# Performance work log

Hardware: AMD Instinct MI355X
Metric: run time of the kernel (lower is better)

## Reference

```python
import jax, jax.numpy as jnp
import numpy as np

B, T, C = 8, 4096, 384
H, F = 6, 64          # heads, head_size; H*F == C
E = 131072            # edges per graph (shared across batch)
D_FF = 4 * C
NEG_SLOPE = 0.2       # PyG GATConv LeakyReLU slope
EPS = 1e-5


def layer_norm(x, g, b):
    mu = jnp.mean(x, axis=-1, keepdims=True)
    var = jnp.mean(jnp.square(x - mu), axis=-1, keepdims=True)
    return (x - mu) * jax.lax.rsqrt(var + EPS) * g + b


def setup_inputs() -> dict:
    key = jax.random.key(0)
    ks = jax.random.split(key, 14)
    s = 0.02
    return {
        "x": jax.random.normal(ks[0], (B, T, C), dtype=jnp.float32),
        "edge_index": jax.random.randint(ks[1], (2, E), 0, T, dtype=jnp.int32),
        "W_gat": jax.random.normal(ks[2], (C, H * F), dtype=jnp.float32) * s,
        "att_src": jax.random.normal(ks[3], (H, F), dtype=jnp.float32) * s,
        "att_dst": jax.random.normal(ks[4], (H, F), dtype=jnp.float32) * s,
        "b_gat": jnp.zeros((C,), dtype=jnp.float32),
        "ln1_g": jnp.ones((C,), dtype=jnp.float32),
        "ln1_b": jnp.zeros((C,), dtype=jnp.float32),
        "ln2_g": jnp.ones((C,), dtype=jnp.float32),
        "ln2_b": jnp.zeros((C,), dtype=jnp.float32),
        "W1": jax.random.normal(ks[5], (C, D_FF), dtype=jnp.float32) * s,
        "b1": jnp.zeros((D_FF,), dtype=jnp.float32),
        "W2": jax.random.normal(ks[6], (D_FF, C), dtype=jnp.float32) * s,
        "b2": jnp.zeros((C,), dtype=jnp.float32),
    }


def reference(x, edge_index, W_gat, att_src, att_dst, b_gat,
              ln1_g, ln1_b, ln2_g, ln2_b, W1, b1, W2, b2):
    # PyG GATConv adds self-loops by default
    loop = jnp.arange(T, dtype=edge_index.dtype)
    src = jnp.concatenate([edge_index[0], loop])  # [E+T]
    dst = jnp.concatenate([edge_index[1], loop])  # [E+T]

    def gat_single(xn):  # xn: [T, C] (already layer-normed)
        h = (xn @ W_gat).reshape(T, H, F)                      # [T,H,F]
        a_src = jnp.einsum('thf,hf->th', h, att_src)           # [T,H]
        a_dst = jnp.einsum('thf,hf->th', h, att_dst)           # [T,H]
        alpha = a_src[src] + a_dst[dst]                        # [E+T,H]
        alpha = jnp.where(alpha >= 0, alpha, NEG_SLOPE * alpha)
        # segment softmax over incoming edges of each dst node
        m = jax.ops.segment_max(alpha, dst, num_segments=T)    # [T,H]
        ex = jnp.exp(alpha - m[dst])
        denom = jax.ops.segment_sum(ex, dst, num_segments=T)   # [T,H]
        w = ex / denom[dst]                                    # [E+T,H]
        msg = w[:, :, None] * h[src]                           # [E+T,H,F]
        out = jax.ops.segment_sum(msg, dst, num_segments=T)    # [T,H,F]
        return out.reshape(T, H * F) + b_gat

    out = jax.vmap(gat_single)(layer_norm(x, ln1_g, ln1_b))    # [B,T,C]
    x = x + out                                                # dropout in eval mode = identity
    h = layer_norm(x, ln2_g, ln2_b)
    x = x + (jnp.maximum(h @ W1 + b1, 0.0) @ W2 + b2)
    return x
```

## Files before the change

### kernel.cpp

```cpp
#include <hip/hip_runtime.h>
#include <hip/hip_bf16.h>

#define Bb 8
#define Tt 4096
#define Cc 384
#define Hh 6
#define Ee 131072
#define DFF 1536
#define NROWS (Bb * Tt)
#define NEG_SLOPE 0.2f

typedef short bf16x8 __attribute__((ext_vector_type(8)));
typedef float f32x4 __attribute__((ext_vector_type(4)));

__device__ inline float bf2f(unsigned short u) {
    union { unsigned int i; float f; } x; x.i = ((unsigned int)u) << 16; return x.f;
}
__device__ inline unsigned short f2bf(float f) {
    union { float f; unsigned int i; } x; x.f = f;
    unsigned int r = x.i + 0x7fffu + ((x.i >> 16) & 1u);
    return (unsigned short)(r >> 16);
}
__device__ __forceinline__ float blo(unsigned int u) {
    union { unsigned int i; float f; } x; x.i = u << 16; return x.f;
}
__device__ __forceinline__ float bhi(unsigned int u) {
    union { unsigned int i; float f; } x; x.i = u & 0xffff0000u; return x.f;
}

__device__ __forceinline__ void gl_lds16(const unsigned short* g, unsigned short* l) {
    __builtin_amdgcn_global_load_lds(
        (const __attribute__((address_space(1))) unsigned int*)g,
        (__attribute__((address_space(3))) unsigned int*)l,
        16, 0, 0);
}

__global__ __launch_bounds__(256) void ln_bf16_kernel(const float* __restrict__ x,
                                                      const float* __restrict__ g,
                                                      const float* __restrict__ b,
                                                      unsigned short* __restrict__ y) {
    int row = blockIdx.x * 4 + (threadIdx.x >> 6);
    int lane = threadIdx.x & 63;
    const float* xr = x + (size_t)row * Cc;
    float v[6]; float sum = 0.f, sq = 0.f;
#pragma unroll
    for (int j = 0; j < 6; j++) { float t = xr[j * 64 + lane]; v[j] = t; sum += t; sq += t * t; }
#pragma unroll
    for (int off = 1; off < 64; off <<= 1) { sum += __shfl_xor(sum, off); sq += __shfl_xor(sq, off); }
    float mu = sum * (1.f / 384.f);
    float var = sq * (1.f / 384.f) - mu * mu;
    float rs = rsqrtf(var + 1e-5f);
    unsigned short* yr = y + (size_t)row * Cc;
#pragma unroll
    for (int j = 0; j < 6; j++) { int c = j * 64 + lane; yr[c] = f2bf((v[j] - mu) * rs * g[c] + b[c]); }
}

__global__ __launch_bounds__(256) void transpose_bf16_kernel(const float* __restrict__ W,
                                                             unsigned short* __restrict__ Wt,
                                                             int K, int N) {
    __shared__ float t[32][33];
    const int n0 = blockIdx.x * 32, k0 = blockIdx.y * 32;
    const int tx = threadIdx.x & 31, ty = threadIdx.x >> 5;
#pragma unroll
    for (int dy = 0; dy < 32; dy += 8)
        t[ty + dy][tx] = W[(size_t)(k0 + ty + dy) * N + n0 + tx];
    __syncthreads();
#pragma unroll
    for (int dy = 0; dy < 32; dy += 8)
        Wt[(size_t)(n0 + ty + dy) * K + k0 + tx] = f2bf(t[tx][ty + dy]);
}

__global__ __launch_bounds__(256) void att_kernel(const unsigned short* __restrict__ h,
                                                  const float* __restrict__ att_src,
                                                  const float* __restrict__ att_dst,
                                                  float* __restrict__ asrc,
                                                  float* __restrict__ adst) {
    int row = blockIdx.x * 4 + (threadIdx.x >> 6);
    int lane = threadIdx.x & 63;
    const unsigned short* hr = h + (size_t)row * Cc;
#pragma unroll
    for (int j = 0; j < 6; j++) {
        float v = bf2f(hr[j * 64 + lane]);
        float ps = v * att_src[j * 64 + lane];
        float pd = v * att_dst[j * 64 + lane];
#pragma unroll
        for (int off = 1; off < 64; off <<= 1) { ps += __shfl_xor(ps, off); pd += __shfl_xor(pd, off); }
        if (lane == 0) { asrc[row * Hh + j] = ps; adst[row * Hh + j] = pd; }
    }
}

__global__ void count_kernel(const int* __restrict__ dst, int* __restrict__ deg) {
    int e = blockIdx.x * 256 + threadIdx.x;
    if (e < Ee) atomicAdd(&deg[dst[e]], 1);
}

__global__ __launch_bounds__(1024) void scan_kernel(int* __restrict__ deg_cursor,
                                                    int* __restrict__ rowptr) {
    __shared__ int lds[1024];
    int tid = threadIdx.x;
    int base_i = tid * 4;
    int v[4];
#pragma unroll
    for (int i = 0; i < 4; i++) v[i] = deg_cursor[base_i + i];
    int s = v[0] + v[1] + v[2] + v[3];
    lds[tid] = s;
    __syncthreads();
    for (int off = 1; off < 1024; off <<= 1) {
        int t = 0;
        if (tid >= off) t = lds[tid - off];
        __syncthreads();
        lds[tid] += t;
        __syncthreads();
    }
    int incl = lds[tid];
    int excl = incl - s;
    int r = excl;
#pragma unroll
    for (int i = 0; i < 4; i++) { rowptr[base_i + i] = r; deg_cursor[base_i + i] = r; r += v[i]; }
    if (tid == 1023) rowptr[Tt] = incl;
}

__global__ void scatter_kernel(const int* __restrict__ src, const int* __restrict__ dst,
                               int* __restrict__ cursor, int* __restrict__ csr) {
    int e = blockIdx.x * 256 + threadIdx.x;
    if (e < Ee) {
        int d = dst[e];
        int pos = atomicAdd(&cursor[d], 1);
        csr[pos] = src[e];
    }
}

__global__ __launch_bounds__(256) void gat_kernel(const unsigned short* __restrict__ h,
                                                  const float* __restrict__ asrc,
                                                  const float* __restrict__ adst,
                                                  const int* __restrict__ rowptr,
                                                  const int* __restrict__ csr,
                                                  const float* __restrict__ x,
                                                  const float* __restrict__ bgat,
                                                  const float* __restrict__ ln2g,
                                                  const float* __restrict__ ln2b,
                                                  float* __restrict__ x2,
                                                  unsigned short* __restrict__ xn) {
    __shared__ float lds_ex[4][64 * 6];
    const int wave = threadIdx.x >> 6;
    const int gid = blockIdx.x * 4 + wave;
    const int lane = threadIdx.x & 63;
    const int b = gid >> 12;
    const int t = gid & (Tt - 1);
    const int bt = b * Tt;
    const bool hihalf = (lane & 32) != 0;
    const int wsel = hihalf ? 1 : 0;
    float* exbuf = lds_ex[wave];

    float adst_j[6];
    {
        const float2* adp = (const float2*)(adst + gid * Hh);
        float2 d01 = adp[0], d23 = adp[1], d45 = adp[2];
        adst_j[0] = d01.x; adst_j[1] = d01.y; adst_j[2] = d23.x;
        adst_j[3] = d23.y; adst_j[4] = d45.x; adst_j[5] = d45.y;
    }

    float den[6], exs[6];
    {
        const float2* asp = (const float2*)(asrc + gid * Hh);
        float2 s01 = asp[0], s23 = asp[1], s45 = asp[2];
        float as_[6] = {s01.x, s01.y, s23.x, s23.y, s45.x, s45.y};
#pragma unroll
        for (int j = 0; j < 6; j++) {
            float a = as_[j] + adst_j[j];
            a = (a >= 0.f) ? a : NEG_SLOPE * a;
            exs[j] = __expf(a);
            den[j] = (lane == 0) ? exs[j] : 0.f;
        }
    }
    float acc[3][2];
    {
        const unsigned short* hs = h + (size_t)gid * Cc;
#pragma unroll
        for (int k = 0; k < 3; k++) {
            unsigned int u = *(const unsigned int*)(hs + k * 128 + 2 * lane);
            float w = exs[2 * k + wsel];
            acc[k][0] = w * blo(u);
            acc[k][1] = w * bhi(u);
        }
    }

    const int e0 = rowptr[t], e1 = rowptr[t + 1];
    for (int c0 = e0; c0 < e1; c0 += 64) {
        const int e = c0 + lane;
        const bool valid = e < e1;
        const int s = csr[valid ? e : (e1 - 1)];
        const int nb = bt + s;
        float ex[6];
        {
            const float2* ap = (const float2*)(asrc + nb * Hh);
            float2 a01 = ap[0], a23 = ap[1], a45 = ap[2];
            float al[6] = {a01.x, a01.y, a23.x, a23.y, a45.x, a45.y};
#pragma unroll
            for (int j = 0; j < 6; j++) {
                float a = al[j] + adst_j[j];
                a = (a >= 0.f) ? a : NEG_SLOPE * a;
                float exx = __expf(a);
                ex[j] = valid ? exx : 0.f;
                den[j] += ex[j];
            }
        }
        *(float2*)&exbuf[lane * 6 + 0] = make_float2(ex[0], ex[1]);
        *(float2*)&exbuf[lane * 6 + 2] = make_float2(ex[2], ex[3]);
        *(float2*)&exbuf[lane * 6 + 4] = make_float2(ex[4], ex[5]);

        const int cnt = (e1 - c0 < 64) ? (e1 - c0) : 64;
        int l2 = 0;
        for (; l2 + 8 <= cnt; l2 += 8) {
            unsigned int u[8][3];
#pragma unroll
            for (int q = 0; q < 8; q++) {
                const int sb = __builtin_amdgcn_readlane(s, l2 + q);
                const unsigned short* hr = h + (size_t)(bt + sb) * Cc + 2 * lane;
                u[q][0] = *(const unsigned int*)(hr);
                u[q][1] = *(const unsigned int*)(hr + 128);
                u[q][2] = *(const unsigned int*)(hr + 256);
            }
#pragma unroll
            for (int q = 0; q < 8; q++) {
                const int e6 = (l2 + q) * 6 + wsel;
                const float w0 = exbuf[e6];
                const float w1 = exbuf[e6 + 2];
                const float w2 = exbuf[e6 + 4];
                acc[0][0] = fmaf(w0, blo(u[q][0]), acc[0][0]);
                acc[0][1] = fmaf(w0, bhi(u[q][0]), acc[0][1]);
                acc[1][0] = fmaf(w1, blo(u[q][1]), acc[1][0]);
                acc[1][1] = fmaf(w1, bhi(u[q][1]), acc[1][1]);
                acc[2][0] = fmaf(w2, blo(u[q][2]), acc[2][0]);
                acc[2][1] = fmaf(w2, bhi(u[q][2]), acc[2][1]);
            }
        }
        for (; l2 < cnt; l2++) {
            const int sb = __builtin_amdgcn_readlane(s, l2);
            const unsigned short* hr = h + (size_t)(bt + sb) * Cc + 2 * lane;
            unsigned int u0 = *(const unsigned int*)(hr);
            unsigned int u1 = *(const unsigned int*)(hr + 128);
            unsigned int u2 = *(const unsigned int*)(hr + 256);
            const int e6 = l2 * 6 + wsel;
            const float w0 = exbuf[e6];
            const float w1 = exbuf[e6 + 2];
            const float w2 = exbuf[e6 + 4];
            acc[0][0] = fmaf(w0, blo(u0), acc[0][0]);
            acc[0][1] = fmaf(w0, bhi(u0), acc[0][1]);
            acc[1][0] = fmaf(w1, blo(u1), acc[1][0]);
            acc[1][1] = fmaf(w1, bhi(u1), acc[1][1]);
            acc[2][0] = fmaf(w2, blo(u2), acc[2][0]);
            acc[2][1] = fmaf(w2, bhi(u2), acc[2][1]);
        }
    }

#pragma unroll
    for (int j = 0; j < 6; j++)
#pragma unroll
        for (int off = 1; off < 64; off <<= 1) den[j] += __shfl_xor(den[j], off);

    float2 ov[3];
#pragma unroll
    for (int k = 0; k < 3; k++) {
        float d = hihalf ? den[2 * k + 1] : den[2 * k];
        float inv = 1.0f / d;
        const int chan = k * 128 + 2 * lane;
        const size_t idx = (size_t)gid * Cc + chan;
        const float2 bg = *(const float2*)(bgat + chan);
        const float2 xv = *(const float2*)(x + idx);
        ov[k].x = fmaf(acc[k][0], inv, bg.x + xv.x);
        ov[k].y = fmaf(acc[k][1], inv, bg.y + xv.y);
        *(float2*)(x2 + idx) = ov[k];
    }
    float sum = 0.f, sq = 0.f;
#pragma unroll
    for (int k = 0; k < 3; k++) {
        sum += ov[k].x + ov[k].y;
        sq += ov[k].x * ov[k].x + ov[k].y * ov[k].y;
    }
#pragma unroll
    for (int off = 1; off < 64; off <<= 1) { sum += __shfl_xor(sum, off); sq += __shfl_xor(sq, off); }
    const float mu = sum * (1.f / 384.f);
    const float var = sq * (1.f / 384.f) - mu * mu;
    const float rs = rsqrtf(var + 1e-5f);
#pragma unroll
    for (int k = 0; k < 3; k++) {
        const int chan = k * 128 + 2 * lane;
        const size_t idx = (size_t)gid * Cc + chan;
        const float2 gg = *(const float2*)(ln2g + chan);
        const float2 bb = *(const float2*)(ln2b + chan);
        float y0 = (ov[k].x - mu) * rs * gg.x + bb.x;
        float y1 = (ov[k].y - mu) * rs * gg.y + bb.y;
        unsigned int pack = (unsigned int)f2bf(y0) | ((unsigned int)f2bf(y1) << 16);
        *(unsigned int*)(xn + idx) = pack;
    }
}

template <int EPI>
__global__ __launch_bounds__(256, 3) void mfma_gemm(const unsigned short* __restrict__ A,
                                                    const unsigned short* __restrict__ Bt,
                                                    const float* __restrict__ bias,
                                                    const float* __restrict__ resid,
                                                    void* __restrict__ Cout,
                                                    int M, int N, int K) {
    __shared__ unsigned short Als[2 * 128 * 32];
    __shared__ unsigned short Bls[2 * 128 * 32];
    const int tid = threadIdx.x;
    const int wave = tid >> 6, lane = tid & 63;
    const int quad = lane >> 4, l16 = lane & 15;
    const int wm = (wave >> 1) * 64, wn = (wave & 1) * 64;
    const int bm = blockIdx.y, bn = blockIdx.x;

    const int c0 = wave * 2;
    const int rowin = lane >> 2;
    const int kel = (lane & 3) * 8;

    const unsigned short* ga = A + (size_t)(bm * 128 + c0 * 16 + rowin) * K + kel;
    const unsigned short* gb = Bt + (size_t)(bn * 128 + c0 * 16 + rowin) * K + kel;
    unsigned short* la = Als + c0 * 512;
    unsigned short* lb = Bls + c0 * 512;

    f32x4 acc[4][4] = {};

    for (int k0 = 0; k0 < K; k0 += 64) {
        gl_lds16(ga + k0, la);
        gl_lds16(ga + k0 + (size_t)16 * K, la + 512);
        gl_lds16(ga + k0 + 32, la + 4096);
        gl_lds16(ga + k0 + (size_t)16 * K + 32, la + 4096 + 512);
        gl_lds16(gb + k0, lb);
        gl_lds16(gb + k0 + (size_t)16 * K, lb + 512);
        gl_lds16(gb + k0 + 32, lb + 4096);
        gl_lds16(gb + k0 + (size_t)16 * K + 32, lb + 4096 + 512);
        __syncthreads();
#pragma unroll
        for (int hh = 0; hh < 2; hh++) {
            bf16x8 af[4], bfr[4];
#pragma unroll
            for (int i = 0; i < 4; i++) {
                af[i]  = *(const bf16x8*)(Als + hh * 4096 + (wm + i * 16 + l16) * 32 + quad * 8);
                bfr[i] = *(const bf16x8*)(Bls + hh * 4096 + (wn + i * 16 + l16) * 32 + quad * 8);
            }
#pragma unroll
            for (int i = 0; i < 4; i++)
#pragma unroll
                for (int j = 0; j < 4; j++)
                    acc[i][j] = __builtin_amdgcn_mfma_f32_16x16x32_bf16(af[i], bfr[j], acc[i][j], 0, 0, 0);
        }
        __syncthreads();
    }

    const int gm = bm * 128 + wm + quad * 4;
    const int gn = bn * 128 + wn + l16;
#pragma unroll
    for (int i = 0; i < 4; i++) {
#pragma unroll
        for (int j = 0; j < 4; j++) {
            const int col = gn + j * 16;
            const float bv = (EPI == 1 || EPI == 2) ? bias[col] : 0.f;
#pragma unroll
            for (int r = 0; r < 4; r++) {
                const int row = gm + i * 16 + r;
                float v = acc[i][j][r] + bv;
                if constexpr (EPI == 1) {
                    ((unsigned short*)Cout)[(size_t)row * N + col] = f2bf(fmaxf(v, 0.f));
                } else if constexpr (EPI == 2) {
                    ((float*)Cout)[(size_t)row * N + col] = v + resid[(size_t)row * N + col];
                } else if constexpr (EPI == 3) {
                    ((unsigned short*)Cout)[(size_t)row * N + col] = f2bf(v);
                } else {
                    ((float*)Cout)[(size_t)row * N + col] = v;
                }
            }
        }
    }
}

extern "C" void kernel_launch(void* const* d_in, const int* in_sizes, int n_in,
                              void* d_out, int out_size, void* d_ws, size_t ws_size,
                              hipStream_t stream) {
    (void)in_sizes; (void)n_in; (void)out_size; (void)ws_size;
    const float* x      = (const float*)d_in[0];
    const int*   ei     = (const int*)d_in[1];
    const float* Wgat   = (const float*)d_in[2];
    const float* attsrc = (const float*)d_in[3];
    const float* attdst = (const float*)d_in[4];
    const float* bgat   = (const float*)d_in[5];
    const float* ln1g   = (const float*)d_in[6];
    const float* ln1b   = (const float*)d_in[7];
    const float* ln2g   = (const float*)d_in[8];
    const float* ln2b   = (const float*)d_in[9];
    const float* W1     = (const float*)d_in[10];
    const float* b1     = (const float*)d_in[11];
    const float* W2     = (const float*)d_in[12];
    const float* b2     = (const float*)d_in[13];
    float* out = (float*)d_out;

    const int* srcp = ei;
    const int* dstp = ei + Ee;

    char* p = (char*)d_ws;
    unsigned short* xn = (unsigned short*)p; p += (size_t)NROWS * Cc * 2;
    unsigned short* h = (unsigned short*)p; p += (size_t)NROWS * Cc * 2;
    float* asrc = (float*)p; p += (size_t)NROWS * Hh * 4;
    float* adst = (float*)p; p += (size_t)NROWS * Hh * 4;
    unsigned short* ffn1 = (unsigned short*)p; p += (size_t)NROWS * DFF * 2;
    unsigned short* wgt = (unsigned short*)p; p += (size_t)Cc * Cc * 2;
    unsigned short* w1t = (unsigned short*)p; p += (size_t)DFF * Cc * 2;
    unsigned short* w2t = (unsigned short*)p; p += (size_t)Cc * DFF * 2;
    int* rowptr = (int*)p; p += (Tt + 1) * 4;
    int* cursor = (int*)p; p += Tt * 4;
    int* csr = (int*)p; p += (size_t)Ee * 4;

    transpose_bf16_kernel<<<dim3(Cc / 32, Cc / 32), 256, 0, stream>>>(Wgat, wgt, Cc, Cc);
    transpose_bf16_kernel<<<dim3(DFF / 32, Cc / 32), 256, 0, stream>>>(W1, w1t, Cc, DFF);
    transpose_bf16_kernel<<<dim3(Cc / 32, DFF / 32), 256, 0, stream>>>(W2, w2t, DFF, Cc);

    hipMemsetAsync(cursor, 0, Tt * sizeof(int), stream);
    count_kernel<<<(Ee + 255) / 256, 256, 0, stream>>>(dstp, cursor);
    scan_kernel<<<1, 1024, 0, stream>>>(cursor, rowptr);
    scatter_kernel<<<(Ee + 255) / 256, 256, 0, stream>>>(srcp, dstp, cursor, csr);

    ln_bf16_kernel<<<NROWS / 4, 256, 0, stream>>>(x, ln1g, ln1b, xn);
    mfma_gemm<3><<<dim3(Cc / 128, NROWS / 128), 256, 0, stream>>>(
        xn, wgt, nullptr, nullptr, h, NROWS, Cc, Cc);
    att_kernel<<<NROWS / 4, 256, 0, stream>>>(h, attsrc, attdst, asrc, adst);
    gat_kernel<<<NROWS / 4, 256, 0, stream>>>(h, asrc, adst, rowptr, csr, x, bgat,
                                              ln2g, ln2b, out, xn);
    mfma_gemm<1><<<dim3(DFF / 128, NROWS / 128), 256, 0, stream>>>(
        xn, w1t, b1, nullptr, ffn1, NROWS, DFF, Cc);
    mfma_gemm<2><<<dim3(Cc / 128, NROWS / 128), 256, 0, stream>>>(
        ffn1, w2t, b2, out, out, NROWS, Cc, DFF);
}
```

Measured before the change: 414.4 us.

## Fold attention projections into LN1 and process two nodes per wave in GAT

Precomputes W_gat·att_src/att_dst into a 384x12 matrix so the attention logits come out of the first layer-norm kernel, which removes the separate att_kernel pass over h. The GAT aggregation kernel now gives each half-wave one destination node, so a wave handles two nodes. Each iteration issues gathers for both nodes' neighbour rows, meant to raise memory-level parallelism and halve the wave count. The trade-offs are wasted lanes when the two nodes' degrees differ, and logits computed from bf16 LN output rather than from bf16 h, a small numerical difference.

```diff
diff --git a/kernel.cpp b/kernel.cpp
--- a/kernel.cpp
+++ b/kernel.cpp
@@ -35,6 +35,74 @@
         16, 0, 0);
 }
 
+__global__ void wcomb_kernel(const float* __restrict__ Wgat,
+                             const float* __restrict__ att_src,
+                             const float* __restrict__ att_dst,
+                             float* __restrict__ Wcomb) {
+    int t = blockIdx.x * 256 + threadIdx.x;
+    if (t >= 384 * 12) return;
+    int k = t / 12, j = t % 12;
+    int hd = j % 6;
+    const float* av = (j < 6 ? att_src : att_dst) + hd * 64;
+    const float* wr = Wgat + (size_t)k * Cc + hd * 64;
+    float acc = 0.f;
+#pragma unroll 8
+    for (int f = 0; f < 64; f++) acc = fmaf(wr[f], av[f], acc);
+    Wcomb[k * 12 + j] = acc;
+}
+
+__global__ __launch_bounds__(256) void ln1_att_kernel(const float* __restrict__ x,
+                                                      const float* __restrict__ g,
+                                                      const float* __restrict__ b,
+                                                      const float* __restrict__ Wcomb,
+                                                      unsigned short* __restrict__ y,
+                                                      float* __restrict__ asrc,
+                                                      float* __restrict__ adst) {
+    int row = blockIdx.x * 4 + (threadIdx.x >> 6);
+    int lane = threadIdx.x & 63;
+    const float* xr = x + (size_t)row * Cc;
+    float v[6]; float sum = 0.f, sq = 0.f;
+#pragma unroll
+    for (int j = 0; j < 6; j++) { float t = xr[j * 64 + lane]; v[j] = t; sum += t; sq += t * t; }
+#pragma unroll
+    for (int off = 1; off < 64; off <<= 1) { sum += __shfl_xor(sum, off); sq += __shfl_xor(sq, off); }
+    float mu = sum * (1.f / 384.f);
+    float var = sq * (1.f / 384.f) - mu * mu;
+    float rs = rsqrtf(var + 1e-5f);
+    unsigned short* yr = y + (size_t)row * Cc;
+    float p[12];
+#pragma unroll
+    for (int jj = 0; jj < 12; jj++) p[jj] = 0.f;
+#pragma unroll
+    for (int j = 0; j < 6; j++) {
+        int c = j * 64 + lane;
+        float yv = (v[j] - mu) * rs * g[c] + b[c];
+        unsigned short ub = f2bf(yv);
+        yr[c] = ub;
+        float yq = bf2f(ub);
+        const float4* w = (const float4*)(Wcomb + c * 12);
+        float4 w0 = w[0], w1 = w[1], w2 = w[2];
+        p[0] = fmaf(yq, w0.x, p[0]); p[1] = fmaf(yq, w0.y, p[1]);
+        p[2] = fmaf(yq, w0.z, p[2]); p[3] = fmaf(yq, w0.w, p[3]);
+        p[4] = fmaf(yq, w1.x, p[4]); p[5] = fmaf(yq, w1.y, p[5]);
+        p[6] = fmaf(yq, w1.z, p[6]); p[7] = fmaf(yq, w1.w, p[7]);
+        p[8] = fmaf(yq, w2.x, p[8]); p[9] = fmaf(yq, w2.y, p[9]);
+        p[10] = fmaf(yq, w2.z, p[10]); p[11] = fmaf(yq, w2.w, p[11]);
+    }
+#pragma unroll
+    for (int off = 1; off < 64; off <<= 1)
+#pragma unroll
+        for (int jj = 0; jj < 12; jj++) p[jj] += __shfl_xor(p[jj], off);
+    if (lane == 0) {
+        float* as_ = asrc + row * Hh;
+        float* ad_ = adst + row * Hh;
+        as_[0] = p[0]; as_[1] = p[1]; as_[2] = p[2];
+        as_[3] = p[3]; as_[4] = p[4]; as_[5] = p[5];
+        ad_[0] = p[6]; ad_[1] = p[7]; ad_[2] = p[8];
+        ad_[3] = p[9]; ad_[4] = p[10]; ad_[5] = p[11];
+    }
+}
+
 __global__ __launch_bounds__(256) void ln_bf16_kernel(const float* __restrict__ x,
                                                       const float* __restrict__ g,
                                                       const float* __restrict__ b,
@@ -68,25 +136,6 @@
 #pragma unroll
     for (int dy = 0; dy < 32; dy += 8)
         Wt[(size_t)(n0 + ty + dy) * K + k0 + tx] = f2bf(t[tx][ty + dy]);
-}
-
-__global__ __launch_bounds__(256) void att_kernel(const unsigned short* __restrict__ h,
-                                                  const float* __restrict__ att_src,
-                                                  const float* __restrict__ att_dst,
-                                                  float* __restrict__ asrc,
-                                                  float* __restrict__ adst) {
-    int row = blockIdx.x * 4 + (threadIdx.x >> 6);
-    int lane = threadIdx.x & 63;
-    const unsigned short* hr = h + (size_t)row * Cc;
-#pragma unroll
-    for (int j = 0; j < 6; j++) {
-        float v = bf2f(hr[j * 64 + lane]);
-        float ps = v * att_src[j * 64 + lane];
-        float pd = v * att_dst[j * 64 + lane];
-#pragma unroll
-        for (int off = 1; off < 64; off <<= 1) { ps += __shfl_xor(ps, off); pd += __shfl_xor(pd, off); }
-        if (lane == 0) { asrc[row * Hh + j] = ps; adst[row * Hh + j] = pd; }
-    }
 }
 
 __global__ void count_kernel(const int* __restrict__ dst, int* __restrict__ deg) {
@@ -143,53 +192,81 @@
                                                   unsigned short* __restrict__ xn) {
     __shared__ float lds_ex[4][64 * 6];
     const int wave = threadIdx.x >> 6;
-    const int gid = blockIdx.x * 4 + wave;
     const int lane = threadIdx.x & 63;
-    const int b = gid >> 12;
-    const int t = gid & (Tt - 1);
-    const int bt = b * Tt;
-    const bool hihalf = (lane & 32) != 0;
+    const int wid = blockIdx.x * 4 + wave;
+    const int gidA = wid * 2;
+    const int gidB = gidA + 1;
+    const int bt = gidA & ~(Tt - 1);
+    const int tA = gidA & (Tt - 1);
+    const int halflane = lane & 31;
+    const bool isB = lane >= 32;
+    const bool hihalf = isB;
     const int wsel = hihalf ? 1 : 0;
     float* exbuf = lds_ex[wave];
 
-    float adst_j[6];
+    float adA[6], adB[6];
     {
-        const float2* adp = (const float2*)(adst + gid * Hh);
-        float2 d01 = adp[0], d23 = adp[1], d45 = adp[2];
-        adst_j[0] = d01.x; adst_j[1] = d01.y; adst_j[2] = d23.x;
-        adst_j[3] = d23.y; adst_j[4] = d45.x; adst_j[5] = d45.y;
-    }
-
-    float den[6], exs[6];
+        const float2* pA = (const float2*)(adst + gidA * Hh);
+        const float2* pB = (const float2*)(adst + gidB * Hh);
+        float2 a0 = pA[0], a1 = pA[1], a2 = pA[2];
+        float2 b0 = pB[0], b1 = pB[1], b2 = pB[2];
+        adA[0] = a0.x; adA[1] = a0.y; adA[2] = a1.x; adA[3] = a1.y; adA[4] = a2.x; adA[5] = a2.y;
+        adB[0] = b0.x; adB[1] = b0.y; adB[2] = b1.x; adB[3] = b1.y; adB[4] = b2.x; adB[5] = b2.y;
+    }
+    float exsA[6], exsB[6];
     {
-        const float2* asp = (const float2*)(asrc + gid * Hh);
-        float2 s01 = asp[0], s23 = asp[1], s45 = asp[2];
-        float as_[6] = {s01.x, s01.y, s23.x, s23.y, s45.x, s45.y};
+        const float2* pA = (const float2*)(asrc + gidA * Hh);
+        const float2* pB = (const float2*)(asrc + gidB * Hh);
+        float2 a0 = pA[0], a1 = pA[1], a2 = pA[2];
+        float2 b0 = pB[0], b1 = pB[1], b2 = pB[2];
+        float sA[6] = {a0.x, a0.y, a1.x, a1.y, a2.x, a2.y};
+        float sB[6] = {b0.x, b0.y, b1.x, b1.y, b2.x, b2.y};
 #pragma unroll
         for (int j = 0; j < 6; j++) {
-            float a = as_[j] + adst_j[j];
+            float a = sA[j] + adA[j];
             a = (a >= 0.f) ? a : NEG_SLOPE * a;
-            exs[j] = __expf(a);
-            den[j] = (lane == 0) ? exs[j] : 0.f;
-        }
-    }
-    float acc[3][2];
+            exsA[j] = __expf(a);
+            float c = sB[j] + adB[j];
+            c = (c >= 0.f) ? c : NEG_SLOPE * c;
+            exsB[j] = __expf(c);
+        }
+    }
+    float den[6];
+#pragma unroll
+    for (int j = 0; j < 6; j++)
+        den[j] = (lane == 0) ? exsA[j] : ((lane == 32) ? exsB[j] : 0.f);
+
+    float accA[3][2], accB[3][2];
     {
-        const unsigned short* hs = h + (size_t)gid * Cc;
+        const unsigned short* hA = h + (size_t)gidA * Cc + 2 * lane;
+        const unsigned short* hB = h + (size_t)gidB * Cc + 2 * lane;
 #pragma unroll
         for (int k = 0; k < 3; k++) {
-            unsigned int u = *(const unsigned int*)(hs + k * 128 + 2 * lane);
-            float w = exs[2 * k + wsel];
-            acc[k][0] = w * blo(u);
-            acc[k][1] = w * bhi(u);
-        }
-    }
-
-    const int e0 = rowptr[t], e1 = rowptr[t + 1];
-    for (int c0 = e0; c0 < e1; c0 += 64) {
-        const int e = c0 + lane;
-        const bool valid = e < e1;
-        const int s = csr[valid ? e : (e1 - 1)];
+            unsigned int uA = *(const unsigned int*)(hA + k * 128);
+            unsigned int uB = *(const unsigned int*)(hB + k * 128);
+            float wA = exsA[2 * k + wsel];
+            float wB = exsB[2 * k + wsel];
+            accA[k][0] = wA * blo(uA); accA[k][1] = wA * bhi(uA);
+            accB[k][0] = wB * blo(uB); accB[k][1] = wB * bhi(uB);
+        }
+    }
+
+    const int e0A = rowptr[tA], e1A = rowptr[tA + 1], e1B = rowptr[tA + 2];
+    const int e0B = e1A;
+    const int cntA = e1A - e0A, cntB = e1B - e0B;
+    const int maxcnt = cntA > cntB ? cntA : cntB;
+    const int my_e0 = isB ? e0B : e0A;
+    const int my_e1 = isB ? e1B : e1A;
+    float adM[6];
+#pragma unroll
+    for (int j = 0; j < 6; j++) adM[j] = isB ? adB[j] : adA[j];
+
+    for (int c = 0; c < maxcnt; c += 32) {
+        const int e = my_e0 + c + halflane;
+        const bool valid = e < my_e1;
+        int eidx = valid ? e : (my_e1 - 1);
+        eidx = eidx < 0 ? 0 : eidx;
+        const int s = csr[eidx];
         const int nb = bt + s;
         float ex[6];
         {
@@ -198,7 +275,7 @@
             float al[6] = {a01.x, a01.y, a23.x, a23.y, a45.x, a45.y};
 #pragma unroll
             for (int j = 0; j < 6; j++) {
-                float a = al[j] + adst_j[j];
+                float a = al[j] + adM[j];
                 a = (a >= 0.f) ? a : NEG_SLOPE * a;
                 float exx = __expf(a);
                 ex[j] = valid ? exx : 0.f;
@@ -209,90 +286,122 @@
         *(float2*)&exbuf[lane * 6 + 2] = make_float2(ex[2], ex[3]);
         *(float2*)&exbuf[lane * 6 + 4] = make_float2(ex[4], ex[5]);
 
-        const int cnt = (e1 - c0 < 64) ? (e1 - c0) : 64;
-        int l2 = 0;
-        for (; l2 + 8 <= cnt; l2 += 8) {
-            unsigned int u[8][3];
-#pragma unroll
-            for (int q = 0; q < 8; q++) {
-                const int sb = __builtin_amdgcn_readlane(s, l2 + q);
-                const unsigned short* hr = h + (size_t)(bt + sb) * Cc + 2 * lane;
-                u[q][0] = *(const unsigned int*)(hr);
-                u[q][1] = *(const unsigned int*)(hr + 128);
-                u[q][2] = *(const unsigned int*)(hr + 256);
+        const int rem = maxcnt - c;
+        const int cntc = rem < 32 ? rem : 32;
+        int q = 0;
+        for (; q + 4 <= cntc; q += 4) {
+            unsigned int u[4][6];
+#pragma unroll
+            for (int p = 0; p < 4; p++) {
+                const int sbA = __builtin_amdgcn_readlane(s, q + p);
+                const int sbB = __builtin_amdgcn_readlane(s, 32 + q + p);
+                const unsigned short* hA = h + (size_t)(bt + sbA) * Cc + 2 * lane;
+                const unsigned short* hB = h + (size_t)(bt + sbB) * Cc + 2 * lane;
+                u[p][0] = *(const unsigned int*)(hA);
+                u[p][1] = *(const unsigned int*)(hA + 128);
+                u[p][2] = *(const unsigned int*)(hA + 256);
+                u[p][3] = *(const unsigned int*)(hB);
+                u[p][4] = *(const unsigned int*)(hB + 128);
+                u[p][5] = *(const unsigned int*)(hB + 256);
             }
 #pragma unroll
-            for (int q = 0; q < 8; q++) {
-                const int e6 = (l2 + q) * 6 + wsel;
-                const float w0 = exbuf[e6];
-                const float w1 = exbuf[e6 + 2];
-                const float w2 = exbuf[e6 + 4];
-                acc[0][0] = fmaf(w0, blo(u[q][0]), acc[0][0]);
-                acc[0][1] = fmaf(w0, bhi(u[q][0]), acc[0][1]);
-                acc[1][0] = fmaf(w1, blo(u[q][1]), acc[1][0]);
-                acc[1][1] = fmaf(w1, bhi(u[q][1]), acc[1][1]);
-                acc[2][0] = fmaf(w2, blo(u[q][2]), acc[2][0]);
-                acc[2][1] = fmaf(w2, bhi(u[q][2]), acc[2][1]);
+            for (int p = 0; p < 4; p++) {
+                const int eA = (q + p) * 6 + wsel;
+                const int eB = eA + 192;
+                const float wA0 = exbuf[eA], wA1 = exbuf[eA + 2], wA2 = exbuf[eA + 4];
+                const float wB0 = exbuf[eB], wB1 = exbuf[eB + 2], wB2 = exbuf[eB + 4];
+                accA[0][0] = fmaf(wA0, blo(u[p][0]), accA[0][0]);
+                accA[0][1] = fmaf(wA0, bhi(u[p][0]), accA[0][1]);
+                accA[1][0] = fmaf(wA1, blo(u[p][1]), accA[1][0]);
+                accA[1][1] = fmaf(wA1, bhi(u[p][1]), accA[1][1]);
+                accA[2][0] = fmaf(wA2, blo(u[p][2]), accA[2][0]);
+                accA[2][1] = fmaf(wA2, bhi(u[p][2]), accA[2][1]);
+                accB[0][0] = fmaf(wB0, blo(u[p][3]), accB[0][0]);
+                accB[0][1] = fmaf(wB0, bhi(u[p][3]), accB[0][1]);
+                accB[1][0] = fmaf(wB1, blo(u[p][4]), accB[1][0]);
+                accB[1][1] = fmaf(wB1, bhi(u[p][4]), accB[1][1]);
+                accB[2][0] = fmaf(wB2, blo(u[p][5]), accB[2][0]);
+                accB[2][1] = fmaf(wB2, bhi(u[p][5]), accB[2][1]);
             }
         }
-        for (; l2 < cnt; l2++) {
-            const int sb = __builtin_amdgcn_readlane(s, l2);
-            const unsigned short* hr = h + (size_t)(bt + sb) * Cc + 2 * lane;
-            unsigned int u0 = *(const unsigned int*)(hr);
-            unsigned int u1 = *(const unsigned int*)(hr + 128);
-            unsigned int u2 = *(const unsigned int*)(hr + 256);
-            const int e6 = l2 * 6 + wsel;
-            const float w0 = exbuf[e6];
-            const float w1 = exbuf[e6 + 2];
-            const float w2 = exbuf[e6 + 4];
-            acc[0][0] = fmaf(w0, blo(u0), acc[0][0]);
-            acc[0][1] = fmaf(w0, bhi(u0), acc[0][1]);
-            acc[1][0] = fmaf(w1, blo(u1), acc[1][0]);
-            acc[1][1] = fmaf(w1, bhi(u1), acc[1][1]);
-            acc[2][0] = fmaf(w2, blo(u2), acc[2][0]);
-            acc[2][1] = fmaf(w2, bhi(u2), acc[2][1]);
+        for (; q < cntc; q++) {
+            const int sbA = __builtin_amdgcn_readlane(s, q);
+            const int sbB = __builtin_amdgcn_readlane(s, 32 + q);
+            const unsigned short* hA = h + (size_t)(bt + sbA) * Cc + 2 * lane;
+            const unsigned short* hB = h + (size_t)(bt + sbB) * Cc + 2 * lane;
+            unsigned int u0 = *(const unsigned int*)(hA);
+            unsigned int u1 = *(const unsigned int*)(hA + 128);
+            unsigned int u2 = *(const unsigned int*)(hA + 256);
+            unsigned int u3 = *(const unsigned int*)(hB);
+            unsigned int u4 = *(const unsigned int*)(hB + 128);
+            unsigned int u5 = *(const unsigned int*)(hB + 256);
+            const int eA = q * 6 + wsel;
+            const int eB = eA + 192;
+            const float wA0 = exbuf[eA], wA1 = exbuf[eA + 2], wA2 = exbuf[eA + 4];
+            const float wB0 = exbuf[eB], wB1 = exbuf[eB + 2], wB2 = exbuf[eB + 4];
+            accA[0][0] = fmaf(wA0, blo(u0), accA[0][0]);
+            accA[0][1] = fmaf(wA0, bhi(u0), accA[0][1]);
+            accA[1][0] = fmaf(wA1, blo(u1), accA[1][0]);
+            accA[1][1] = fmaf(wA1, bhi(u1), accA[1][1]);
+            accA[2][0] = fmaf(wA2, blo(u2), accA[2][0]);
+            accA[2][1] = fmaf(wA2, bhi(u2), accA[2][1]);
+            accB[0][0] = fmaf(wB0, blo(u3), accB[0][0]);
+            accB[0][1] = fmaf(wB0, bhi(u3), accB[0][1]);
+            accB[1][0] = fmaf(wB1, blo(u4), accB[1][0]);
+            accB[1][1] = fmaf(wB1, bhi(u4), accB[1][1]);
+            accB[2][0] = fmaf(wB2, blo(u5), accB[2][0]);
+            accB[2][1] = fmaf(wB2, bhi(u5), accB[2][1]);
         }
     }
 
 #pragma unroll
     for (int j = 0; j < 6; j++)
 #pragma unroll
-        for (int off = 1; off < 64; off <<= 1) den[j] += __shfl_xor(den[j], off);
-
-    float2 ov[3];
-#pragma unroll
-    for (int k = 0; k < 3; k++) {
-        float d = hihalf ? den[2 * k + 1] : den[2 * k];
-        float inv = 1.0f / d;
-        const int chan = k * 128 + 2 * lane;
-        const size_t idx = (size_t)gid * Cc + chan;
-        const float2 bg = *(const float2*)(bgat + chan);
-        const float2 xv = *(const float2*)(x + idx);
-        ov[k].x = fmaf(acc[k][0], inv, bg.x + xv.x);
-        ov[k].y = fmaf(acc[k][1], inv, bg.y + xv.y);
-        *(float2*)(x2 + idx) = ov[k];
-    }
-    float sum = 0.f, sq = 0.f;
-#pragma unroll
-    for (int k = 0; k < 3; k++) {
-        sum += ov[k].x + ov[k].y;
-        sq += ov[k].x * ov[k].x + ov[k].y * ov[k].y;
-    }
-#pragma unroll
-    for (int off = 1; off < 64; off <<= 1) { sum += __shfl_xor(sum, off); sq += __shfl_xor(sq, off); }
-    const float mu = sum * (1.f / 384.f);
-    const float var = sq * (1.f / 384.f) - mu * mu;
-    const float rs = rsqrtf(var + 1e-5f);
-#pragma unroll
-    for (int k = 0; k < 3; k++) {
-        const int chan = k * 128 + 2 * lane;
-        const size_t idx = (size_t)gid * Cc + chan;
-        const float2 gg = *(const float2*)(ln2g + chan);
-        const float2 bb = *(const float2*)(ln2b + chan);
-        float y0 = (ov[k].x - mu) * rs * gg.x + bb.x;
-        float y1 = (ov[k].y - mu) * rs * gg.y + bb.y;
-        unsigned int pack = (unsigned int)f2bf(y0) | ((unsigned int)f2bf(y1) << 16);
-        *(unsigned int*)(xn + idx) = pack;
+        for (int off = 1; off < 32; off <<= 1) den[j] += __shfl_xor(den[j], off);
+    float denA[6], denB[6];
+#pragma unroll
+    for (int j = 0; j < 6; j++) { denA[j] = __shfl(den[j], 0); denB[j] = __shfl(den[j], 32); }
+
+#pragma unroll
+    for (int nd = 0; nd < 2; nd++) {
+        const int gid = nd ? gidB : gidA;
+        float2 ov[3];
+#pragma unroll
+        for (int k = 0; k < 3; k++) {
+            float d = nd ? denB[2 * k + wsel] : denA[2 * k + wsel];
+            float inv = 1.0f / d;
+            float a0 = nd ? accB[k][0] : accA[k][0];
+            float a1 = nd ? accB[k][1] : accA[k][1];
+            const int chan = k * 128 + 2 * lane;
+            const size_t idx = (size_t)gid * Cc + chan;
+            const float2 bg = *(const float2*)(bgat + chan);
+            const float2 xv = *(const float2*)(x + idx);
+            ov[k].x = fmaf(a0, inv, bg.x + xv.x);
+            ov[k].y = fmaf(a1, inv, bg.y + xv.y);
+            *(float2*)(x2 + idx) = ov[k];
+        }
+        float sum = 0.f, sq = 0.f;
+#pragma unroll
+        for (int k = 0; k < 3; k++) {
+            sum += ov[k].x + ov[k].y;
+            sq += ov[k].x * ov[k].x + ov[k].y * ov[k].y;
+        }
+#pragma unroll
+        for (int off = 1; off < 64; off <<= 1) { sum += __shfl_xor(sum, off); sq += __shfl_xor(sq, off); }
+        const float mu = sum * (1.f / 384.f);
+        const float var = sq * (1.f / 384.f) - mu * mu;
+        const float rs = rsqrtf(var + 1e-5f);
+#pragma unroll
+        for (int k = 0; k < 3; k++) {
+            const int chan = k * 128 + 2 * lane;
+            const size_t idx = (size_t)gid * Cc + chan;
+            const float2 gg = *(const float2*)(ln2g + chan);
+            const float2 bb = *(const float2*)(ln2b + chan);
+            float y0 = (ov[k].x - mu) * rs * gg.x + bb.x;
+            float y1 = (ov[k].y - mu) * rs * gg.y + bb.y;
+            unsigned int pack = (unsigned int)f2bf(y0) | ((unsigned int)f2bf(y1) << 16);
+            *(unsigned int*)(xn + idx) = pack;
+        }
     }
 }
 
@@ -407,6 +516,7 @@
     unsigned short* wgt = (unsigned short*)p; p += (size_t)Cc * Cc * 2;
     unsigned short* w1t = (unsigned short*)p; p += (size_t)DFF * Cc * 2;
     unsigned short* w2t = (unsigned short*)p; p += (size_t)Cc * DFF * 2;
+    float* wcomb = (float*)p; p += (size_t)Cc * 12 * 4;
     int* rowptr = (int*)p; p += (Tt + 1) * 4;
     int* cursor = (int*)p; p += Tt * 4;
     int* csr = (int*)p; p += (size_t)Ee * 4;
@@ -414,17 +524,17 @@
     transpose_bf16_kernel<<<dim3(Cc / 32, Cc / 32), 256, 0, stream>>>(Wgat, wgt, Cc, Cc);
     transpose_bf16_kernel<<<dim3(DFF / 32, Cc / 32), 256, 0, stream>>>(W1, w1t, Cc, DFF);
     transpose_bf16_kernel<<<dim3(Cc / 32, DFF / 32), 256, 0, stream>>>(W2, w2t, DFF, Cc);
+    wcomb_kernel<<<18, 256, 0, stream>>>(Wgat, attsrc, attdst, wcomb);
 
     hipMemsetAsync(cursor, 0, Tt * sizeof(int), stream);
     count_kernel<<<(Ee + 255) / 256, 256, 0, stream>>>(dstp, cursor);
     scan_kernel<<<1, 1024, 0, stream>>>(cursor, rowptr);
     scatter_kernel<<<(Ee + 255) / 256, 256, 0, stream>>>(srcp, dstp, cursor, csr);
 
-    ln_bf16_kernel<<<NROWS / 4, 256, 0, stream>>>(x, ln1g, ln1b, xn);
+    ln1_att_kernel<<<NROWS / 4, 256, 0, stream>>>(x, ln1g, ln1b, wcomb, xn, asrc, adst);
     mfma_gemm<3><<<dim3(Cc / 128, NROWS / 128), 256, 0, stream>>>(
         xn, wgt, nullptr, nullptr, h, NROWS, Cc, Cc);
-    att_kernel<<<NROWS / 4, 256, 0, stream>>>(h, attsrc, attdst, asrc, adst);
-    gat_kernel<<<NROWS / 4, 256, 0, stream>>>(h, asrc, adst, rowptr, csr, x, bgat,
+    gat_kernel<<<NROWS / 8, 256, 0, stream>>>(h, asrc, adst, rowptr, csr, x, bgat,
                                               ln2g, ln2b, out, xn);
     mfma_gemm<1><<<dim3(DFF / 128, NROWS / 128), 256, 0, stream>>>(
         xn, w1t, b1, nullptr, ffn1, NROWS, DFF, Cc);
```

New measurement: 405.0 us. 2.3% less time.
